# Performance work log

Hardware: AMD Instinct MI355X
Metric: run time of the kernel (lower is better)

Reference implementation:

```python
import jax, jax.numpy as jnp
import numpy as np

V = 1024          # vocab_size
N = 500_000       # num automaton states
A = 16            # arcs per non-start state (start state has V dense arcs)
MAX_ORDER = 4     # max n-gram order -> max backoff chain length
START = 0         # start (unigram) state
B = 8192          # batch of hypotheses


def _build_automaton(seed=0):
    rng = np.random.default_rng(seed)
    num_arcs = V + (N - 1) * A
    arcs_weights = -(rng.random(num_arcs).astype(np.float32) * 8.0 + 0.05)
    to_states = rng.integers(0, N, num_arcs).astype(np.int32)
    ilabels = np.empty(num_arcs, np.int32)
    ilabels[:V] = np.arange(V, dtype=np.int32)  # start state: arc index == ilabel
    # unique sorted ilabels per non-start state
    base = rng.integers(0, V, N - 1).astype(np.int32)
    offs = np.arange(A, dtype=np.int32) * (V // A)
    ilabels[V:] = np.sort((base[:, None] + offs[None, :]) % V, axis=1).reshape(-1)
    state_start = np.empty(N, np.int32)
    state_end = np.empty(N, np.int32)
    state_start[0] = 0
    state_end[0] = V
    state_start[1:] = V + np.arange(N - 1, dtype=np.int32) * A
    state_end[1:] = state_start[1:] + A
    # state orders: start=1, rest in 2..MAX_ORDER; backoff goes to an order-(k-1) state
    order = np.empty(N, np.int64)
    order[0] = 1
    order[1:] = rng.integers(2, MAX_ORDER + 1, N - 1)
    order[1:MAX_ORDER] = np.arange(2, MAX_ORDER + 1)  # guarantee each order nonempty
    backoff_to = np.zeros(N, np.int32)               # order-2 states back off to START
    for k in range(3, MAX_ORDER + 1):
        mask = order == k
        prev = np.flatnonzero(order == k - 1)
        backoff_to[mask] = rng.choice(prev, mask.sum()).astype(np.int32)
    backoff_weights = -(rng.random(N).astype(np.float32) * 3.0)
    backoff_weights[0] = 0.0
    return dict(
        arcs_weights=jnp.asarray(arcs_weights),
        backoff_weights=jnp.asarray(backoff_weights),
        ilabels=jnp.asarray(ilabels),
        to_states=jnp.asarray(to_states),
        backoff_to_states=jnp.asarray(backoff_to),
        state_start_arcs=jnp.asarray(state_start),
        state_end_arcs=jnp.asarray(state_end),
    )


def setup_inputs() -> dict:
    key = jax.random.key(0)
    inp = _build_automaton(0)
    inp["states"] = jax.random.randint(key, (B,), 0, N, dtype=jnp.int32)
    return inp


def _advance(states, arcs_weights, backoff_weights, ilabels, to_states,
             backoff_to_states, state_start_arcs, state_end_arcs):
    b = states.shape[0]
    rows = jnp.arange(b)[:, None]
    # column V is a dump slot for masked-out scatters
    scores_e = jnp.zeros((b, V + 1), arcs_weights.dtype)
    next_e = jnp.zeros((b, V + 1), jnp.int32)
    found_e = jnp.zeros((b, V + 1), bool)
    cur = states.astype(jnp.int32)
    acc = jnp.zeros((b,), arcs_weights.dtype)  # accumulated backoff weight
    offs = jnp.arange(A, dtype=jnp.int32)
    for _ in range(MAX_ORDER - 1):  # chase backoffs down to the start state
        at_start = cur == START
        idx = state_start_arcs[cur][:, None] + offs                    # [b, A]
        valid = (idx < state_end_arcs[cur][:, None]) & (~at_start)[:, None]
        idx = jnp.where(valid, idx, 0)
        lab = ilabels[idx]                                             # [b, A]
        can = valid & ~jnp.take_along_axis(found_e, lab, axis=1)
        slot = jnp.where(can, lab, V)
        scores_e = scores_e.at[rows, slot].set(acc[:, None] + arcs_weights[idx])
        next_e = next_e.at[rows, slot].set(to_states[idx])
        found_e = found_e.at[rows, slot].set(True)
        acc = jnp.where(at_start, acc, acc + backoff_weights[cur])
        cur = jnp.where(at_start, cur, backoff_to_states[cur])
    # start state has a dense arc table: arc index == ilabel for 0..V-1
    nf = ~found_e[:, :V]
    scores = jnp.where(nf, acc[:, None] + arcs_weights[None, :V], scores_e[:, :V])
    next_states = jnp.where(nf, to_states[None, :V], next_e[:, :V])
    return scores, next_states


def reference(states, arcs_weights, backoff_weights, ilabels, to_states,
              backoff_to_states, state_start_arcs, state_end_arcs):
    return _advance(states, arcs_weights, backoff_weights, ilabels, to_states,
                    backoff_to_states, state_start_arcs, state_end_arcs)
```

## Files before the change

### kernel.cpp

```cpp
#include <hip/hip_runtime.h>

#define VOCAB 1024
#define ARCS  16
#define CHAIN 3
#define START_STATE 0
#define WAVE 64
#define WAVES_PER_BLOCK 4
#define BLOCK (WAVE * WAVES_PER_BLOCK)
#define NCHUNK (VOCAB / (WAVE * 4))

typedef float f32x4 __attribute__((ext_vector_type(4)));
typedef int   i32x4 __attribute__((ext_vector_type(4)));

__global__ __launch_bounds__(BLOCK, 5) void ngram_advance_kernel(
    const float* __restrict__ arcs_weights,
    const float* __restrict__ backoff_weights,
    const int*   __restrict__ ilabels,
    const int*   __restrict__ to_states,
    const int*   __restrict__ backoff_to,
    const int*   __restrict__ state_start,
    const int*   __restrict__ state_end,
    const int*   __restrict__ states,
    float*       __restrict__ out_scores,
    float*       __restrict__ out_next,
    int B)
{
    __shared__ int   s_next[WAVES_PER_BLOCK][VOCAB];
    __shared__ float s_sc  [WAVES_PER_BLOCK][VOCAB];

    const int lane = threadIdx.x & (WAVE - 1);
    const int wid  = __builtin_amdgcn_readfirstlane(threadIdx.x >> 6);
    const int b    = blockIdx.x * WAVES_PER_BLOCK + wid;
    if (b >= B) return;

    int*   __restrict__ ovn = s_next[wid];
    float* __restrict__ ovs = s_sc[wid];

    int cur = states[b];

    #pragma unroll
    for (int i = 0; i < NCHUNK; ++i)
        *(i32x4*)&ovn[(lane + i * WAVE) * 4] = (i32x4){-1, -1, -1, -1};

    f32x4 rn[NCHUNK], dw[NCHUNK];
    #pragma unroll
    for (int i = 0; i < NCHUNK; ++i) {
        const int v = (lane + i * WAVE) * 4;
        const i32x4 dn = *(const i32x4*)&to_states[v];
        rn[i].x = (float)dn.x; rn[i].y = (float)dn.y;
        rn[i].z = (float)dn.z; rn[i].w = (float)dn.w;
        dw[i] = *(const f32x4*)&arcs_weights[v];
    }

    float acc = 0.0f;
    const int   cs0 = cur;  const float ca0 = acc;
    acc += backoff_weights[cur];  cur = backoff_to[cur];
    const int   cs1 = cur;  const float ca1 = acc;
    acc += backoff_weights[cur];  cur = backoff_to[cur];
    const int   cs2 = cur;  const float ca2 = acc;
    acc += backoff_weights[cur];
    const float accf = acc;

    const int level = lane >> 4;
    const int arc   = lane & (ARCS - 1);
    int   lab = -1, ns = 0;
    float sc  = 0.0f;
    bool  ok  = false;
    if (lane < CHAIN * ARCS) {
        const int   s    = (level == 0) ? cs0 : (level == 1) ? cs1 : cs2;
        const float cacc = (level == 0) ? ca0 : (level == 1) ? ca1 : ca2;
        if (s != START_STATE) {
            const int idx = state_start[s] + arc;
            if (idx < state_end[s]) {
                lab = ilabels[idx];
                sc  = cacc + arcs_weights[idx];
                ns  = to_states[idx];
                ok  = true;
            }
        }
    }

    if (ok && level == 2) { ovs[lab] = sc; ovn[lab] = ns; }
    __builtin_amdgcn_sched_barrier(0);
    if (ok && level == 1) { ovs[lab] = sc; ovn[lab] = ns; }
    __builtin_amdgcn_sched_barrier(0);
    if (ok && level == 0) { ovs[lab] = sc; ovn[lab] = ns; }
    __builtin_amdgcn_sched_barrier(0);

    float* __restrict__ so = out_scores + (size_t)b * VOCAB;
    float* __restrict__ no = out_next   + (size_t)b * VOCAB;
    #pragma unroll
    for (int i = 0; i < NCHUNK; ++i) {
        const int v = (lane + i * WAVE) * 4;
        const i32x4 on = *(const i32x4*)&ovn[v];
        const f32x4 os = *(const f32x4*)&ovs[v];
        f32x4 rs, rx;
        rs.x = (on.x >= 0) ? os.x : accf + dw[i].x;
        rs.y = (on.y >= 0) ? os.y : accf + dw[i].y;
        rs.z = (on.z >= 0) ? os.z : accf + dw[i].z;
        rs.w = (on.w >= 0) ? os.w : accf + dw[i].w;
        rx.x = (on.x >= 0) ? (float)on.x : rn[i].x;
        rx.y = (on.y >= 0) ? (float)on.y : rn[i].y;
        rx.z = (on.z >= 0) ? (float)on.z : rn[i].z;
        rx.w = (on.w >= 0) ? (float)on.w : rn[i].w;
        *(f32x4*)&so[v] = rs;
        *(f32x4*)&no[v] = rx;
    }
}

extern "C" void kernel_launch(void* const* d_in, const int* in_sizes, int n_in,
                              void* d_out, int out_size, void* d_ws, size_t ws_size,
                              hipStream_t stream) {
    const float* arcs_weights    = (const float*)d_in[0];
    const float* backoff_weights = (const float*)d_in[1];
    const int*   ilabels         = (const int*)d_in[2];
    const int*   to_states       = (const int*)d_in[3];
    const int*   backoff_to      = (const int*)d_in[4];
    const int*   state_start     = (const int*)d_in[5];
    const int*   state_end       = (const int*)d_in[6];
    const int*   states          = (const int*)d_in[7];

    const int B = in_sizes[7];
    float* out_scores = (float*)d_out;
    float* out_next   = out_scores + (size_t)B * VOCAB;

    const int grid = (B + WAVES_PER_BLOCK - 1) / WAVES_PER_BLOCK;
    ngram_advance_kernel<<<grid, BLOCK, 0, stream>>>(
        arcs_weights, backoff_weights, ilabels, to_states, backoff_to,
        state_start, state_end, states, out_scores, out_next, B);
}
```

Measured before the change: 19.55 us.

## Store owner lane bytes in LDS and fetch overrides via ds_bpermute

Each vocabulary slot now keeps a one-byte record of which lane holds its override, replacing the per-wave float and int override tables, and values are pulled from the owning lane with ds_bpermute. The dense start-state arc loads move into the output loop instead of being held in registers. This cuts LDS from 32 KB to 4 KB per block and lowers register pressure, so the occupancy hint rises from 5 to 8. In exchange it issues 32 extra bpermute operations per lane and reloads the dense arrays inside the store loop.

```diff
diff --git a/kernel.cpp b/kernel.cpp
--- a/kernel.cpp
+++ b/kernel.cpp
@@ -12,7 +12,7 @@
 typedef float f32x4 __attribute__((ext_vector_type(4)));
 typedef int   i32x4 __attribute__((ext_vector_type(4)));
 
-__global__ __launch_bounds__(BLOCK, 5) void ngram_advance_kernel(
+__global__ __launch_bounds__(BLOCK, 8) void ngram_advance_kernel(
     const float* __restrict__ arcs_weights,
     const float* __restrict__ backoff_weights,
     const int*   __restrict__ ilabels,
@@ -25,32 +25,18 @@
     float*       __restrict__ out_next,
     int B)
 {
-    __shared__ int   s_next[WAVES_PER_BLOCK][VOCAB];
-    __shared__ float s_sc  [WAVES_PER_BLOCK][VOCAB];
+    __shared__ unsigned char s_who[WAVES_PER_BLOCK][VOCAB];
 
     const int lane = threadIdx.x & (WAVE - 1);
     const int wid  = __builtin_amdgcn_readfirstlane(threadIdx.x >> 6);
     const int b    = blockIdx.x * WAVES_PER_BLOCK + wid;
     if (b >= B) return;
 
-    int*   __restrict__ ovn = s_next[wid];
-    float* __restrict__ ovs = s_sc[wid];
+    unsigned char* __restrict__ who = s_who[wid];
 
     int cur = states[b];
 
-    #pragma unroll
-    for (int i = 0; i < NCHUNK; ++i)
-        *(i32x4*)&ovn[(lane + i * WAVE) * 4] = (i32x4){-1, -1, -1, -1};
-
-    f32x4 rn[NCHUNK], dw[NCHUNK];
-    #pragma unroll
-    for (int i = 0; i < NCHUNK; ++i) {
-        const int v = (lane + i * WAVE) * 4;
-        const i32x4 dn = *(const i32x4*)&to_states[v];
-        rn[i].x = (float)dn.x; rn[i].y = (float)dn.y;
-        rn[i].z = (float)dn.z; rn[i].w = (float)dn.w;
-        dw[i] = *(const f32x4*)&arcs_weights[v];
-    }
+    *(i32x4*)&who[lane * 16] = (i32x4){-1, -1, -1, -1};
 
     float acc = 0.0f;
     const int   cs0 = cur;  const float ca0 = acc;
@@ -63,8 +49,8 @@
 
     const int level = lane >> 4;
     const int arc   = lane & (ARCS - 1);
-    int   lab = -1, ns = 0;
-    float sc  = 0.0f;
+    int   lab = -1;
+    float sc  = 0.0f, fns = 0.0f;
     bool  ok  = false;
     if (lane < CHAIN * ARCS) {
         const int   s    = (level == 0) ? cs0 : (level == 1) ? cs1 : cs2;
@@ -74,35 +60,41 @@
             if (idx < state_end[s]) {
                 lab = ilabels[idx];
                 sc  = cacc + arcs_weights[idx];
-                ns  = to_states[idx];
+                fns = (float)to_states[idx];
                 ok  = true;
             }
         }
     }
 
-    if (ok && level == 2) { ovs[lab] = sc; ovn[lab] = ns; }
+    if (ok && level == 2) who[lab] = (unsigned char)lane;
     __builtin_amdgcn_sched_barrier(0);
-    if (ok && level == 1) { ovs[lab] = sc; ovn[lab] = ns; }
+    if (ok && level == 1) who[lab] = (unsigned char)lane;
     __builtin_amdgcn_sched_barrier(0);
-    if (ok && level == 0) { ovs[lab] = sc; ovn[lab] = ns; }
+    if (ok && level == 0) who[lab] = (unsigned char)lane;
     __builtin_amdgcn_sched_barrier(0);
 
     float* __restrict__ so = out_scores + (size_t)b * VOCAB;
     float* __restrict__ no = out_next   + (size_t)b * VOCAB;
+    const int sci = __float_as_int(sc);
+    const int nsi = __float_as_int(fns);
     #pragma unroll
     for (int i = 0; i < NCHUNK; ++i) {
         const int v = (lane + i * WAVE) * 4;
-        const i32x4 on = *(const i32x4*)&ovn[v];
-        const f32x4 os = *(const f32x4*)&ovs[v];
+        const unsigned w4 = *(const unsigned*)&who[v];
+        const f32x4 dwv = *(const f32x4*)&arcs_weights[v];
+        const i32x4 dnv = *(const i32x4*)&to_states[v];
         f32x4 rs, rx;
-        rs.x = (on.x >= 0) ? os.x : accf + dw[i].x;
-        rs.y = (on.y >= 0) ? os.y : accf + dw[i].y;
-        rs.z = (on.z >= 0) ? os.z : accf + dw[i].z;
-        rs.w = (on.w >= 0) ? os.w : accf + dw[i].w;
-        rx.x = (on.x >= 0) ? (float)on.x : rn[i].x;
-        rx.y = (on.y >= 0) ? (float)on.y : rn[i].y;
-        rx.z = (on.z >= 0) ? (float)on.z : rn[i].z;
-        rx.w = (on.w >= 0) ? (float)on.w : rn[i].w;
+        #pragma unroll
+        for (int j = 0; j < 4; ++j) {
+            const unsigned wb = (w4 >> (8 * j)) & 0xFFu;
+            const float scv = __int_as_float(
+                __builtin_amdgcn_ds_bpermute((int)(wb << 2), sci));
+            const float nsv = __int_as_float(
+                __builtin_amdgcn_ds_bpermute((int)(wb << 2), nsi));
+            const bool hit = (wb != 0xFFu);
+            rs[j] = hit ? scv : accf + dwv[j];
+            rx[j] = hit ? nsv : (float)dnv[j];
+        }
         *(f32x4*)&so[v] = rs;
         *(f32x4*)&no[v] = rx;
     }
```

After: 19.38 us. About the same (-0.9%).
